# Kernel tuning notes

Hardware: AMD Instinct MI355X
Metric: run time of the kernel (lower is better)

## Reference

```python
import jax, jax.numpy as jnp
import numpy as np

EPS = 1e-8
TEMP = 0.2
HOPS = 2


def _inv_sqrt_deg(deg):
    # deg^-0.5 with inf -> 0 (isolated nodes)
    return jnp.where(deg > 0, jax.lax.rsqrt(jnp.maximum(deg, 1.0)) * jnp.where(deg > 0, 1.0, 0.0), 0.0)


def gcn_conv(h, u, v, W, b, n):
    # PyG GCNConv: add self-loops, symmetric normalization, aggr='add'
    h = h @ W  # [N, out]
    loops = jnp.arange(n, dtype=u.dtype)
    uu = jnp.concatenate([u, loops])
    vv = jnp.concatenate([v, loops])
    deg = jax.ops.segment_sum(jnp.ones_like(vv, dtype=h.dtype), vv, num_segments=n)
    dis = _inv_sqrt_deg(deg)
    norm = dis[uu] * dis[vv]  # [E+N]
    out = jax.ops.segment_sum(norm[:, None] * h[uu], vv, num_segments=n)
    return out + b


def compute_message_passing(u, v, x, n, hop=HOPS):
    # to_undirected: concat edges with their flips; remove self-loops via mask
    uu = jnp.concatenate([u, v])
    vv = jnp.concatenate([v, u])
    mask = (uu != vv).astype(x.dtype)
    deg = jax.ops.segment_sum(mask, vv, num_segments=n)
    dis = _inv_sqrt_deg(deg)
    norm = dis[uu] * dis[vv] * mask  # zero out self-loop edges
    for _ in range(hop):
        x = jax.ops.segment_sum(norm[:, None] * x[uu], vv, num_segments=n)
    return x


def _cos_sim(a, b):
    na = jnp.maximum(jnp.sqrt(jnp.sum(a * a, axis=-1)), EPS)
    nb = jnp.maximum(jnp.sqrt(jnp.sum(b * b, axis=-1)), EPS)
    return jnp.sum(a * b, axis=-1) / (na * nb)


def setup_inputs() -> dict:
    key = jax.random.key(0)
    ks = jax.random.split(key, 10)
    N, E, B = 100_000, 800_000, 100_000
    Din, H, Dout = 256, 256, 64
    x = jax.random.normal(ks[0], (N, Din), dtype=jnp.float32)
    src = jax.random.randint(ks[1], (E,), 0, N, dtype=jnp.int32)
    off = jax.random.randint(ks[2], (E,), 1, N, dtype=jnp.int32)
    dst = (src + off) % N  # guaranteed no self-loops
    edge_index = jnp.stack([src, dst])  # [2, E]
    batch = jax.random.randint(ks[3], (B, 3), 0, N, dtype=jnp.int32)
    s1, s2, sp = 1.0 / np.sqrt(Din), 1.0 / np.sqrt(H), 1.0 / np.sqrt(H)
    W1 = jax.random.normal(ks[4], (Din, H), dtype=jnp.float32) * s1
    b1 = jnp.zeros((H,), jnp.float32)
    W2 = jax.random.normal(ks[5], (H, H), dtype=jnp.float32) * s2
    b2 = jnp.zeros((H,), jnp.float32)
    Wp = jax.random.normal(ks[6], (H, Dout), dtype=jnp.float32) * sp
    bp = jnp.zeros((Dout,), jnp.float32)
    return {"x": x, "edge_index": edge_index, "batch": batch,
            "W1": W1, "b1": b1, "W2": W2, "b2": b2, "Wp": Wp, "bp": bp}


def reference(x, edge_index, batch, W1, b1, W2, b2, Wp, bp):
    n = x.shape[0]
    u, v = edge_index[0], edge_index[1]
    # gnn_encoder: 2-layer GCN
    h = jax.nn.relu(gcn_conv(x, u, v, W1, b1, n))
    h = gcn_conv(h, u, v, W2, b2, n)
    # graph_pred_linear
    node_emb = h @ Wp + bp  # [N, Dout]
    # 2-hop degree-normalized propagation on the undirected graph
    all_emb = compute_message_passing(u, v, node_emb, n)
    anc = all_emb[batch[:, 0]]
    pos = all_emb[batch[:, 1]]
    neg = all_emb[batch[:, 2]]
    xs = jnp.exp(_cos_sim(anc, pos) / TEMP)
    ys = jnp.exp(_cos_sim(anc, neg) / TEMP)
    loss = -jnp.log(xs / (xs + ys))
    return loss.mean()
```

## Files before the change

kernel.cpp:

```cpp
#include <hip/hip_runtime.h>
#include <hip/hip_bf16.h>

#define DIN 256
#define HID 256
#define DOUT 64
#define NPART 8
#define FPB 128
#define CCAP 32

typedef short short8 __attribute__((ext_vector_type(8)));
typedef float f32x4 __attribute__((ext_vector_type(4)));
typedef float f32x2 __attribute__((ext_vector_type(2)));

__device__ __forceinline__ float b2f(ushort u) {
    unsigned int x = ((unsigned int)u) << 16;
    return __builtin_bit_cast(float, x);
}
__device__ __forceinline__ ushort f2bf(float f) {
    unsigned int u = __builtin_bit_cast(unsigned int, f);
    unsigned int r = (u + 0x7FFFu + ((u >> 16) & 1u)) >> 16;
    return (ushort)r;
}
__device__ __forceinline__ unsigned int cvt_pk(float lo, float hi) {
    unsigned int r;
    asm("v_cvt_pk_bf16_f32 %0, %1, %2" : "=v"(r) : "v"(lo), "v"(hi));
    return r;
}
__device__ __forceinline__ unsigned char f2fp8(float v) {
    int p = __builtin_amdgcn_cvt_pk_fp8_f32(v, v, 0, false);
    return (unsigned char)(p & 0xff);
}
__device__ __forceinline__ ushort f2fp8x2(float lo, float hi) {
    int p = __builtin_amdgcn_cvt_pk_fp8_f32(lo, hi, 0, false);
    return (ushort)(p & 0xffff);
}
__device__ __forceinline__ void gload16(const void* g, void* l) {
    __builtin_amdgcn_global_load_lds(
        (const __attribute__((address_space(1))) unsigned int*)g,
        (__attribute__((address_space(3))) unsigned int*)l, 16, 0, 0);
}
__device__ __forceinline__ int swz8(int lane, int r) {
    return (((lane >> 1) ^ (r & 7)) << 4) + (lane & 1) * 8;
}

__device__ __forceinline__ void fill_body(int fid,
                                          const int* __restrict__ u,
                                          const int* __restrict__ v,
                                          int* __restrict__ cnt_in,
                                          int* __restrict__ cnt_out,
                                          int* __restrict__ col_in,
                                          int* __restrict__ col_out,
                                          int E, unsigned pdiv) {
    const int part = fid & (NPART - 1);
    const int step = FPB * 512;
    int e = (fid >> 3) * 512 + threadIdx.x;

#define PROC(aa, bb)                                                  \
    do {                                                              \
        if ((unsigned)(bb) / pdiv == (unsigned)part) {                \
            int s_ = atomicAdd(&cnt_in[bb], 1);                       \
            if (s_ < CCAP) col_in[(bb) * CCAP + s_] = (aa);           \
        }                                                             \
        if ((unsigned)(aa) / pdiv == (unsigned)part) {                \
            int s_ = atomicAdd(&cnt_out[aa], 1);                      \
            if (s_ < CCAP) col_out[(aa) * CCAP + s_] = (bb);          \
        }                                                             \
    } while (0)

    for (; e + 3 * step < E; e += 4 * step) {
        int a0 = u[e],            b0 = v[e];
        int a1 = u[e + step],     b1 = v[e + step];
        int a2 = u[e + 2 * step], b2 = v[e + 2 * step];
        int a3 = u[e + 3 * step], b3 = v[e + 3 * step];
        PROC(a0, b0);
        PROC(a1, b1);
        PROC(a2, b2);
        PROC(a3, b3);
    }
    for (; e < E; e += step) {
        int a = u[e], b = v[e];
        PROC(a, b);
    }
#undef PROC
}

template <int NT, int TN, int OUTMODE, bool ADD_BIAS, bool A_F32, bool SCALE>
__device__ __forceinline__ void gemm_body(
    int bidx, char* As, char* Bs,
    const void* __restrict__ A, const char* __restrict__ Bt,
    const float* __restrict__ bias, const float* __restrict__ rowscale,
    void* __restrict__ C, int M) {
    constexpr int BM = 64;
    constexpr int TILES = NT / TN;
    constexpr int FM = (TN == 128) ? 2 : 1;
    constexpr int FN = 2;
    const int tid = threadIdx.x;
    const int w = tid >> 6;
    const int lane = tid & 63;
    const int row0 = bidx * BM;
    const int wrow = (TN == 128) ? ((w >> 2) * 32) : ((w >> 1) * 16);
    const int wcol = (TN == 128) ? ((w & 3) * 32) : ((w & 1) * 32);
    const int g = lane >> 4;
    const int r15 = lane & 15;
    const int wb = w * 1024;

    if (A_F32) {
        const float* Af = (const float*)A;
        int r = tid >> 3;
        int c8 = tid & 7;
        int gr = row0 + r;
        gr = (gr < M) ? gr : (M - 1);
        const float* src = Af + (size_t)gr * 256 + c8 * 8;
#pragma unroll
        for (int k = 0; k < 4; ++k) {
            float4 f0 = *(const float4*)(src + k * 64);
            float4 f1 = *(const float4*)(src + k * 64 + 4);
            uint4 pv;
            pv.x = cvt_pk(f0.x, f0.y);
            pv.y = cvt_pk(f0.z, f0.w);
            pv.z = cvt_pk(f1.x, f1.y);
            pv.w = cvt_pk(f1.z, f1.w);
            int chunk = (c8 + 8 * k) ^ (r & 7);
            *(uint4*)(As + r * 512 + (chunk << 4)) = pv;
        }
    } else {
        const char* gA = (const char*)A + (size_t)row0 * 512;
#pragma unroll
        for (int i = 0; i < BM / 16; ++i)
            gload16(gA + i * 8192 + wb + lane * 16, As + i * 8192 + wb);
    }
    {
        const char* gB = Bt;
#pragma unroll
        for (int i = 0; i < TN / 16; ++i)
            gload16(gB + i * 8192 + wb + lane * 16, Bs + i * 8192 + wb);
    }

#pragma unroll
    for (int t = 0; t < TILES; ++t) {
        __syncthreads();

        f32x4 acc[FM][FN];
#pragma unroll
        for (int m = 0; m < FM; ++m)
#pragma unroll
            for (int n = 0; n < FN; ++n) acc[m][n] = {0.f, 0.f, 0.f, 0.f};

#pragma unroll
        for (int ks = 0; ks < 8; ++ks) {
            short8 a[FM], b[FN];
#pragma unroll
            for (int m = 0; m < FM; ++m) {
                int rl = wrow + m * 16 + r15;
                a[m] = *(const short8*)(As + rl * 512 + (((ks * 4 + g) ^ (rl & 7)) << 4));
            }
#pragma unroll
            for (int n = 0; n < FN; ++n) {
                int cl = wcol + n * 16 + r15;
                b[n] = *(const short8*)(Bs + cl * 512 + (((ks * 4 + g) ^ (cl & 7)) << 4));
            }
#pragma unroll
            for (int m = 0; m < FM; ++m)
#pragma unroll
                for (int n = 0; n < FN; ++n)
                    acc[m][n] = __builtin_amdgcn_mfma_f32_16x16x32_bf16(a[m], b[n], acc[m][n], 0, 0, 0);
        }

        __syncthreads();
        if (t + 1 < TILES) {
            const char* gB = Bt + (size_t)((t + 1) * TN) * 512;
#pragma unroll
            for (int i = 0; i < TN / 16; ++i)
                gload16(gB + i * 8192 + wb + lane * 16, Bs + i * 8192 + wb);
        }

#pragma unroll
        for (int m = 0; m < FM; ++m) {
            int rbase = row0 + wrow + m * 16 + g * 4;
#pragma unroll
            for (int j = 0; j < 4; ++j) {
                int grow = rbase + j;
                if (grow >= M) continue;
                float rs = SCALE ? rowscale[grow] : 1.0f;
#pragma unroll
                for (int n = 0; n < FN; ++n) {
                    int gcol = t * TN + wcol + n * 16 + r15;
                    float vv = acc[m][n][j];
                    if (ADD_BIAS) vv += bias[gcol];
                    if (SCALE) vv *= rs;
                    if (OUTMODE == 2)
                        ((unsigned char*)C)[(size_t)grow * 256 + gcol] = f2fp8(vv);
                    else
                        ((unsigned char*)C)[(size_t)grow * 64 + gcol] = f2fp8(vv);
                }
            }
        }
    }
}

__global__ __launch_bounds__(512) void fill_gemm1_kernel(
    const int* __restrict__ u, const int* __restrict__ v,
    int* __restrict__ cnt_in, int* __restrict__ cnt_out,
    int* __restrict__ col_in, int* __restrict__ col_out,
    int E, unsigned pdiv,
    const float* __restrict__ x, const char* __restrict__ w1t,
    unsigned char* __restrict__ hb, int M,
    int gG, int gF, int nG, int nF) {
    __shared__ __align__(16) char As[64 * 512];
    __shared__ __align__(16) char Bs[64 * 512];
    const int G = blockIdx.x >> 3;
    const int sub = blockIdx.x & 7;
    const int gmin = (gG < gF) ? gG : gF;
    bool isG;
    int idx;
    if (G < 2 * gmin) {
        isG = ((G & 1) == 0);
        idx = (G >> 1) * 8 + sub;
    } else if (gG > gF) {
        isG = true;
        idx = (G - gmin) * 8 + sub;
    } else {
        isG = false;
        idx = (G - gmin) * 8 + sub;
    }
    if (isG) {
        if (idx < nG)
            gemm_body<256, 64, 2, false, true, false>(idx, As, Bs, x, w1t,
                                                      nullptr, nullptr, hb, M);
    } else {
        if (idx < nF)
            fill_body(idx, u, v, cnt_in, cnt_out, col_in, col_out, E, pdiv);
    }
}

template <int NT, int TN, int OUTMODE, bool ADD_BIAS, bool A_F32>
__global__ __launch_bounds__(512) void mfma_gemm_v7(
    const void* __restrict__ A, const char* __restrict__ Bt,
    const float* __restrict__ bias, const float* __restrict__ rowscale,
    void* __restrict__ C, int M) {
    __shared__ __align__(16) char As[64 * 512];
    __shared__ __align__(16) char Bs[TN * 512];
    gemm_body<NT, TN, OUTMODE, ADD_BIAS, A_F32, true>(
        blockIdx.x, As, Bs, A, Bt, bias, rowscale, C, M);
}

__global__ __launch_bounds__(256) void wprep_kernel(
    const float* __restrict__ W1, const float* __restrict__ W2,
    const float* __restrict__ Wp, const float* __restrict__ b2,
    const float* __restrict__ bp,
    char* __restrict__ w1t, char* __restrict__ wct, float* __restrict__ c2) {
    int blk = blockIdx.x;
    int k = threadIdx.x;
    if (blk < 256) {
        int row = blk;
        *(ushort*)(w1t + (size_t)row * 512 + (((k >> 3) ^ (row & 7)) << 4) + (k & 7) * 2)
            = f2bf(W1[k * 256 + row]);
        return;
    }
    if (blk < 320) {
        int c = blk - 256;
        const float* w2row = W2 + (size_t)k * 256;
        float s0 = 0.f, s1 = 0.f, s2 = 0.f, s3 = 0.f;
        float s4 = 0.f, s5 = 0.f, s6 = 0.f, s7 = 0.f;
#pragma unroll 4
        for (int j = 0; j < 256; j += 8) {
            s0 += w2row[j + 0] * Wp[(j + 0) * 64 + c];
            s1 += w2row[j + 1] * Wp[(j + 1) * 64 + c];
            s2 += w2row[j + 2] * Wp[(j + 2) * 64 + c];
            s3 += w2row[j + 3] * Wp[(j + 3) * 64 + c];
            s4 += w2row[j + 4] * Wp[(j + 4) * 64 + c];
            s5 += w2row[j + 5] * Wp[(j + 5) * 64 + c];
            s6 += w2row[j + 6] * Wp[(j + 6) * 64 + c];
            s7 += w2row[j + 7] * Wp[(j + 7) * 64 + c];
        }
        float dot = ((s0 + s1) + (s2 + s3)) + ((s4 + s5) + (s6 + s7));
        *(ushort*)(wct + (size_t)c * 512 + (((k >> 3) ^ (c & 7)) << 4) + (k & 7) * 2)
            = f2bf(dot);
        return;
    }
    if (k < 64) {
        float s = 0.f;
        for (int j = 0; j < 256; ++j) s += b2[j] * Wp[j * 64 + k];
        c2[k] = s + bp[k];
    }
}

__global__ __launch_bounds__(256) void dis_kernel(const int* __restrict__ cnt_in,
                                                  const int* __restrict__ cnt_out,
                                                  float* __restrict__ dis_g,
                                                  float* __restrict__ dis_m,
                                                  int N) {
    int i = blockIdx.x * blockDim.x + threadIdx.x;
    if (i >= N) return;
    int ci = cnt_in[i];
    dis_g[i] = rsqrtf((float)ci + 1.0f);
    int dm = ci + cnt_out[i];
    dis_m[i] = (dm > 0) ? rsqrtf((float)dm) : 0.0f;
}

__global__ __launch_bounds__(256) void conv_gather_fp8(const unsigned char* __restrict__ h,
                                                       const float* __restrict__ dis,
                                                       const float* __restrict__ bias,
                                                       const int* __restrict__ cnt_in,
                                                       const int* __restrict__ col_in,
                                                       char* __restrict__ out,
                                                       int N) {
    int wid = (blockIdx.x * blockDim.x + threadIdx.x) >> 6;
    int lane = threadIdx.x & 63;
    if (wid >= N) return;
    float di = dis[wid];
    float a0, a1, a2, a3;
    {
        unsigned q = *(const unsigned*)(h + (size_t)wid * 256 + lane * 4);
        f32x2 lo = __builtin_amdgcn_cvt_pk_f32_fp8((int)q, false);
        f32x2 hi = __builtin_amdgcn_cvt_pk_f32_fp8((int)q, true);
        a0 = di * lo.x; a1 = di * lo.y; a2 = di * hi.x; a3 = di * hi.y;
    }
    const int* list = col_in + (size_t)wid * CCAP;
    int cnt = cnt_in[wid];
    cnt = (cnt < CCAP) ? cnt : CCAP;
    int e = 0;
    for (; e + 7 < cnt; e += 8) {
        int ss[8];
        unsigned qs[8];
#pragma unroll
        for (int k = 0; k < 8; ++k) ss[k] = list[e + k];
#pragma unroll
        for (int k = 0; k < 8; ++k)
            qs[k] = *(const unsigned*)(h + (size_t)ss[k] * 256 + lane * 4);
#pragma unroll
        for (int k = 0; k < 8; ++k) {
            float wgt = dis[ss[k]];
            f32x2 lo = __builtin_amdgcn_cvt_pk_f32_fp8((int)qs[k], false);
            f32x2 hi = __builtin_amdgcn_cvt_pk_f32_fp8((int)qs[k], true);
            a0 += wgt * lo.x; a1 += wgt * lo.y;
            a2 += wgt * hi.x; a3 += wgt * hi.y;
        }
    }
    for (; e < cnt; ++e) {
        int s = list[e];
        float wgt = dis[s];
        unsigned q = *(const unsigned*)(h + (size_t)s * 256 + lane * 4);
        f32x2 lo = __builtin_amdgcn_cvt_pk_f32_fp8((int)q, false);
        f32x2 hi = __builtin_amdgcn_cvt_pk_f32_fp8((int)q, true);
        a0 += wgt * lo.x; a1 += wgt * lo.y;
        a2 += wgt * hi.x; a3 += wgt * hi.y;
    }
    float4 bv = ((const float4*)bias)[lane];
    float o0 = fmaxf(di * a0 + bv.x, 0.f);
    float o1 = fmaxf(di * a1 + bv.y, 0.f);
    float o2 = fmaxf(di * a2 + bv.z, 0.f);
    float o3 = fmaxf(di * a3 + bv.w, 0.f);
    uint2 ov;
    ov.x = cvt_pk(o0, o1);
    ov.y = cvt_pk(o2, o3);
    *(uint2*)(out + (size_t)wid * 512 + swz8(lane, wid)) = ov;
}

__global__ __launch_bounds__(256) void conv2proj_gather(const unsigned char* __restrict__ q,
                                                        const float* __restrict__ dis_g,
                                                        const float* __restrict__ dis_m,
                                                        const float* __restrict__ c2,
                                                        const int* __restrict__ cnt_in,
                                                        const int* __restrict__ col_in,
                                                        unsigned char* __restrict__ out,
                                                        int N) {
    int wid = (blockIdx.x * blockDim.x + threadIdx.x) >> 6;
    int lane = threadIdx.x & 63;
    if (wid >= N) return;
    const int half = lane >> 5;
    const int l2 = lane & 31;
    const int* list = col_in + (size_t)wid * CCAP;
    int cnt = cnt_in[wid];
    cnt = (cnt < CCAP) ? cnt : CCAP;
    float a0 = 0.f, a1 = 0.f;
    int e = half;
    for (; e + 6 < cnt; e += 8) {
        int s0 = list[e], s1 = list[e + 2], s2 = list[e + 4], s3 = list[e + 6];
        ushort q0 = *(const ushort*)(q + (size_t)s0 * 64 + l2 * 2);
        ushort q1 = *(const ushort*)(q + (size_t)s1 * 64 + l2 * 2);
        ushort q2 = *(const ushort*)(q + (size_t)s2 * 64 + l2 * 2);
        ushort q3 = *(const ushort*)(q + (size_t)s3 * 64 + l2 * 2);
        f32x2 f0 = __builtin_amdgcn_cvt_pk_f32_fp8((int)q0, false);
        f32x2 f1 = __builtin_amdgcn_cvt_pk_f32_fp8((int)q1, false);
        f32x2 f2 = __builtin_amdgcn_cvt_pk_f32_fp8((int)q2, false);
        f32x2 f3 = __builtin_amdgcn_cvt_pk_f32_fp8((int)q3, false);
        a0 += f0.x + f1.x + f2.x + f3.x;
        a1 += f0.y + f1.y + f2.y + f3.y;
    }
    for (; e < cnt; e += 2) {
        int s = list[e];
        ushort qq = *(const ushort*)(q + (size_t)s * 64 + l2 * 2);
        f32x2 f = __builtin_amdgcn_cvt_pk_f32_fp8((int)qq, false);
        a0 += f.x;
        a1 += f.y;
    }
    if (half == 0) {
        ushort qq = *(const ushort*)(q + (size_t)wid * 64 + l2 * 2);
        f32x2 f = __builtin_amdgcn_cvt_pk_f32_fp8((int)qq, false);
        a0 += f.x;
        a1 += f.y;
    }
    a0 += __shfl_xor(a0, 32);
    a1 += __shfl_xor(a1, 32);
    if (half == 0) {
        float dg = dis_g[wid], dm = dis_m[wid];
        float cA = c2[l2 * 2], cB = c2[l2 * 2 + 1];
        *(ushort*)(out + (size_t)wid * 64 + l2 * 2) =
            f2fp8x2(dm * (dg * a0 + cA), dm * (dg * a1 + cB));
    }
}

template <int POW>
__global__ __launch_bounds__(256) void mp_gather_fp8(const unsigned char* __restrict__ in,
                                                     const float* __restrict__ dis,
                                                     const int* __restrict__ cnt_in,
                                                     const int* __restrict__ cnt_out,
                                                     const int* __restrict__ col_in,
                                                     const int* __restrict__ col_out,
                                                     unsigned char* __restrict__ out,
                                                     int N) {
    int wid = (blockIdx.x * blockDim.x + threadIdx.x) >> 6;
    int lane = threadIdx.x & 63;
    if (wid >= N) return;
    const int half = lane >> 5;
    const int l2 = lane & 31;
    const int* list;
    int cnt;
    if (half == 0) {
        list = col_in + (size_t)wid * CCAP;
        cnt = cnt_in[wid];
    } else {
        list = col_out + (size_t)wid * CCAP;
        cnt = cnt_out[wid];
    }
    cnt = (cnt < CCAP) ? cnt : CCAP;
    float a0 = 0.f, a1 = 0.f;
    int e = 0;
    for (; e + 3 < cnt; e += 4) {
        int s0 = list[e], s1 = list[e + 1], s2 = list[e + 2], s3 = list[e + 3];
        ushort q0 = *(const ushort*)(in + (size_t)s0 * 64 + l2 * 2);
        ushort q1 = *(const ushort*)(in + (size_t)s1 * 64 + l2 * 2);
        ushort q2 = *(const ushort*)(in + (size_t)s2 * 64 + l2 * 2);
        ushort q3 = *(const ushort*)(in + (size_t)s3 * 64 + l2 * 2);
        f32x2 f0 = __builtin_amdgcn_cvt_pk_f32_fp8((int)q0, false);
        f32x2 f1 = __builtin_amdgcn_cvt_pk_f32_fp8((int)q1, false);
        f32x2 f2 = __builtin_amdgcn_cvt_pk_f32_fp8((int)q2, false);
        f32x2 f3 = __builtin_amdgcn_cvt_pk_f32_fp8((int)q3, false);
        a0 += f0.x + f1.x + f2.x + f3.x;
        a1 += f0.y + f1.y + f2.y + f3.y;
    }
    for (; e < cnt; ++e) {
        int s = list[e];
        ushort q = *(const ushort*)(in + (size_t)s * 64 + l2 * 2);
        f32x2 f = __builtin_amdgcn_cvt_pk_f32_fp8((int)q, false);
        a0 += f.x;
        a1 += f.y;
    }
    a0 += __shfl_xor(a0, 32);
    a1 += __shfl_xor(a1, 32);
    if (half == 0) {
        float d = dis[wid];
        float sc = (POW == 2) ? d * d : d;
        *(ushort*)(out + (size_t)wid * 64 + l2 * 2) = f2fp8x2(sc * a0, sc * a1);
    }
}

__global__ __launch_bounds__(256) void loss_kernel(const unsigned char* __restrict__ emb,
                                                   const int* __restrict__ batch,
                                                   float* __restrict__ out,
                                                   int B, float invB) {
    const int nhw = gridDim.x * 8;
    const int hwid = blockIdx.x * 8 + (threadIdx.x >> 5);
    const int l2 = threadIdx.x & 31;
    float lsum = 0.0f;
    for (int r = hwid; r < B; r += nhw) {
        int a = batch[r * 3 + 0];
        int p = batch[r * 3 + 1];
        int ng = batch[r * 3 + 2];
        ushort qa = *(const ushort*)(emb + (size_t)a * 64 + l2 * 2);
        ushort qp = *(const ushort*)(emb + (size_t)p * 64 + l2 * 2);
        ushort qn = *(const ushort*)(emb + (size_t)ng * 64 + l2 * 2);
        f32x2 fa = __builtin_amdgcn_cvt_pk_f32_fp8((int)qa, false);
        f32x2 fp = __builtin_amdgcn_cvt_pk_f32_fp8((int)qp, false);
        f32x2 fn = __builtin_amdgcn_cvt_pk_f32_fp8((int)qn, false);
        float aa = fa.x * fa.x + fa.y * fa.y;
        float pp = fp.x * fp.x + fp.y * fp.y;
        float nn = fn.x * fn.x + fn.y * fn.y;
        float ap = fa.x * fp.x + fa.y * fp.y;
        float an = fa.x * fn.x + fa.y * fn.y;
#pragma unroll
        for (int off = 16; off > 0; off >>= 1) {
            aa += __shfl_xor(aa, off);
            pp += __shfl_xor(pp, off);
            nn += __shfl_xor(nn, off);
            ap += __shfl_xor(ap, off);
            an += __shfl_xor(an, off);
        }
        if (l2 == 0) {
            float na = fmaxf(sqrtf(aa), 1e-8f);
            float npp = fmaxf(sqrtf(pp), 1e-8f);
            float nnn = fmaxf(sqrtf(nn), 1e-8f);
            float cx = ap / (na * npp);
            float cy = an / (na * nnn);
            lsum += log1pf(expf((cy - cx) * 5.0f));
        }
    }
    __shared__ float part[8];
    if (l2 == 0) part[threadIdx.x >> 5] = lsum;
    __syncthreads();
    if (threadIdx.x == 0) {
        float s = 0.f;
#pragma unroll
        for (int i = 0; i < 8; ++i) s += part[i];
        atomicAdd(out, s * invB);
    }
}

extern "C" void kernel_launch(void* const* d_in, const int* in_sizes, int n_in,
                              void* d_out, int out_size, void* d_ws, size_t ws_size,
                              hipStream_t stream) {
    const float* x   = (const float*)d_in[0];
    const int* ei    = (const int*)d_in[1];
    const int* batch = (const int*)d_in[2];
    const float* W1  = (const float*)d_in[3];
    const float* b1  = (const float*)d_in[4];
    const float* W2  = (const float*)d_in[5];
    const float* b2  = (const float*)d_in[6];
    const float* Wp  = (const float*)d_in[7];
    const float* bp  = (const float*)d_in[8];
    const int N = in_sizes[0] / DIN;
    const int E = in_sizes[1] / 2;
    const int B = in_sizes[2] / 3;
    const int* u = ei;
    const int* v = ei + E;
    const unsigned pdiv = (unsigned)((N + NPART - 1) / NPART);

    char* aggb    = (char*)d_ws;
    unsigned char* hb = (unsigned char*)(aggb + (size_t)N * 512);
    unsigned char* embA = hb + (size_t)N * 256;
    unsigned char* embB = embA + (size_t)N * 64;
    char* w1t     = (char*)(embB + (size_t)N * 64);
    char* wct     = w1t + 256 * 512;
    float* c2     = (float*)(wct + 64 * 512);
    float* dis_g  = c2 + 64;
    float* dis_m  = dis_g + N;
    int* cnt_in   = (int*)(dis_m + N);
    int* cnt_out  = cnt_in + N;
    int* col_in   = cnt_out + N;
    int* col_out  = col_in + (size_t)N * CCAP;

    const int nwb = (N + 3) / 4;
    const int ndisb = (N + 255) / 256;
    const int gm = (N + 63) / 64;

    hipMemsetAsync(cnt_in, 0, 2 * (size_t)N * sizeof(int), stream);
    wprep_kernel<<<321, 256, 0, stream>>>(W1, W2, Wp, b2, bp, w1t, wct, c2);

    const int nG = gm;
    const int gG = (nG + 7) / 8;
    const int nF = NPART * FPB;
    const int gF = nF / 8;
    fill_gemm1_kernel<<<(gG + gF) * 8, 512, 0, stream>>>(
        u, v, cnt_in, cnt_out, col_in, col_out, E, pdiv,
        x, w1t, hb, N, gG, gF, nG, nF);

    dis_kernel<<<ndisb, 256, 0, stream>>>(cnt_in, cnt_out, dis_g, dis_m, N);

    conv_gather_fp8<<<nwb, 256, 0, stream>>>(hb, dis_g, b1, cnt_in, col_in, aggb, N);

    mfma_gemm_v7<64, 64, 3, false, false><<<gm, 512, 0, stream>>>(
        aggb, wct, nullptr, dis_g, embB, N);

    conv2proj_gather<<<nwb, 256, 0, stream>>>(embB, dis_g, dis_m, c2,
                                              cnt_in, col_in, embA, N);

    mp_gather_fp8<2><<<nwb, 256, 0, stream>>>(embA, dis_m, cnt_in, cnt_out,
                                              col_in, col_out, embB, N);
    mp_gather_fp8<1><<<nwb, 256, 0, stream>>>(embB, dis_m, cnt_in, cnt_out,
                                              col_in, col_out, embA, N);

    hipMemsetAsync(d_out, 0, sizeof(float), stream);
    loss_kernel<<<1024, 256, 0, stream>>>(embA, batch, (float*)d_out, B, 1.0f / (float)B);
}
```

Measured before the change: 372.8 us.

## Compute degree norms on the fly and fold weight prep into fill kernel

Removes the separate dis_kernel and computes rsqrt degree normalizations inline from the count arrays in each gather kernel. The W2·Wp product and bias prep move into extra blocks of the fill/GEMM1 launch, leaving a smaller W1 cast kernel. The row scaling after GEMM2 is moved into conv2proj_gather's per-neighbor weights, so the GEMM epilogue is simpler. Together these drop launches and the dis arrays, at the cost of extra count loads and rsqrt calls in the gathers and a shallower unroll in conv2proj.

```diff
diff --git a/kernel.cpp b/kernel.cpp
--- a/kernel.cpp
+++ b/kernel.cpp
@@ -84,11 +84,10 @@
 #undef PROC
 }
 
-template <int NT, int TN, int OUTMODE, bool ADD_BIAS, bool A_F32, bool SCALE>
+template <int NT, int TN, int OUTMODE, bool A_F32>
 __device__ __forceinline__ void gemm_body(
     int bidx, char* As, char* Bs,
     const void* __restrict__ A, const char* __restrict__ Bt,
-    const float* __restrict__ bias, const float* __restrict__ rowscale,
     void* __restrict__ C, int M) {
     constexpr int BM = 64;
     constexpr int TILES = NT / TN;
@@ -181,13 +180,10 @@
             for (int j = 0; j < 4; ++j) {
                 int grow = rbase + j;
                 if (grow >= M) continue;
-                float rs = SCALE ? rowscale[grow] : 1.0f;
 #pragma unroll
                 for (int n = 0; n < FN; ++n) {
                     int gcol = t * TN + wcol + n * 16 + r15;
                     float vv = acc[m][n][j];
-                    if (ADD_BIAS) vv += bias[gcol];
-                    if (SCALE) vv *= rs;
                     if (OUTMODE == 2)
                         ((unsigned char*)C)[(size_t)grow * 256 + gcol] = f2fp8(vv);
                     else
@@ -205,9 +201,43 @@
     int E, unsigned pdiv,
     const float* __restrict__ x, const char* __restrict__ w1t,
     unsigned char* __restrict__ hb, int M,
+    const float* __restrict__ W2, const float* __restrict__ Wp,
+    const float* __restrict__ b2, const float* __restrict__ bp,
+    char* __restrict__ wct, float* __restrict__ c2,
     int gG, int gF, int nG, int nF) {
     __shared__ __align__(16) char As[64 * 512];
     __shared__ __align__(16) char Bs[64 * 512];
+    const int mainB = (gG + gF) * 8;
+    if ((int)blockIdx.x >= mainB) {
+        int pidx = blockIdx.x - mainB;
+        int k = threadIdx.x & 255;
+        if (pidx < 32) {
+            int c = pidx * 2 + (threadIdx.x >> 8);
+            const float* w2row = W2 + (size_t)k * 256;
+            float s0 = 0.f, s1 = 0.f, s2 = 0.f, s3 = 0.f;
+            float s4 = 0.f, s5 = 0.f, s6 = 0.f, s7 = 0.f;
+#pragma unroll 4
+            for (int j = 0; j < 256; j += 8) {
+                s0 += w2row[j + 0] * Wp[(j + 0) * 64 + c];
+                s1 += w2row[j + 1] * Wp[(j + 1) * 64 + c];
+                s2 += w2row[j + 2] * Wp[(j + 2) * 64 + c];
+                s3 += w2row[j + 3] * Wp[(j + 3) * 64 + c];
+                s4 += w2row[j + 4] * Wp[(j + 4) * 64 + c];
+                s5 += w2row[j + 5] * Wp[(j + 5) * 64 + c];
+                s6 += w2row[j + 6] * Wp[(j + 6) * 64 + c];
+                s7 += w2row[j + 7] * Wp[(j + 7) * 64 + c];
+            }
+            float dot = ((s0 + s1) + (s2 + s3)) + ((s4 + s5) + (s6 + s7));
+            *(ushort*)(wct + (size_t)c * 512 + (((k >> 3) ^ (c & 7)) << 4) + (k & 7) * 2)
+                = f2bf(dot);
+        } else if (threadIdx.x < 64) {
+            int c = threadIdx.x;
+            float s = 0.f;
+            for (int j = 0; j < 256; ++j) s += b2[j] * Wp[j * 64 + c];
+            c2[c] = s + bp[c];
+        }
+        return;
+    }
     const int G = blockIdx.x >> 3;
     const int sub = blockIdx.x & 7;
     const int gmin = (gG < gF) ? gG : gF;
@@ -225,81 +255,31 @@
     }
     if (isG) {
         if (idx < nG)
-            gemm_body<256, 64, 2, false, true, false>(idx, As, Bs, x, w1t,
-                                                      nullptr, nullptr, hb, M);
+            gemm_body<256, 64, 2, true>(idx, As, Bs, x, w1t, hb, M);
     } else {
         if (idx < nF)
             fill_body(idx, u, v, cnt_in, cnt_out, col_in, col_out, E, pdiv);
     }
 }
 
-template <int NT, int TN, int OUTMODE, bool ADD_BIAS, bool A_F32>
-__global__ __launch_bounds__(512) void mfma_gemm_v7(
+template <int NT, int TN, int OUTMODE>
+__global__ __launch_bounds__(512) void mfma_gemm_v8(
     const void* __restrict__ A, const char* __restrict__ Bt,
-    const float* __restrict__ bias, const float* __restrict__ rowscale,
     void* __restrict__ C, int M) {
     __shared__ __align__(16) char As[64 * 512];
     __shared__ __align__(16) char Bs[TN * 512];
-    gemm_body<NT, TN, OUTMODE, ADD_BIAS, A_F32, true>(
-        blockIdx.x, As, Bs, A, Bt, bias, rowscale, C, M);
-}
-
-__global__ __launch_bounds__(256) void wprep_kernel(
-    const float* __restrict__ W1, const float* __restrict__ W2,
-    const float* __restrict__ Wp, const float* __restrict__ b2,
-    const float* __restrict__ bp,
-    char* __restrict__ w1t, char* __restrict__ wct, float* __restrict__ c2) {
-    int blk = blockIdx.x;
+    gemm_body<NT, TN, OUTMODE, false>(blockIdx.x, As, Bs, A, Bt, C, M);
+}
+
+__global__ __launch_bounds__(256) void wcast1_kernel(const float* __restrict__ W1,
+                                                     char* __restrict__ w1t) {
+    int row = blockIdx.x;
     int k = threadIdx.x;
-    if (blk < 256) {
-        int row = blk;
-        *(ushort*)(w1t + (size_t)row * 512 + (((k >> 3) ^ (row & 7)) << 4) + (k & 7) * 2)
-            = f2bf(W1[k * 256 + row]);
-        return;
-    }
-    if (blk < 320) {
-        int c = blk - 256;
-        const float* w2row = W2 + (size_t)k * 256;
-        float s0 = 0.f, s1 = 0.f, s2 = 0.f, s3 = 0.f;
-        float s4 = 0.f, s5 = 0.f, s6 = 0.f, s7 = 0.f;
-#pragma unroll 4
-        for (int j = 0; j < 256; j += 8) {
-            s0 += w2row[j + 0] * Wp[(j + 0) * 64 + c];
-            s1 += w2row[j + 1] * Wp[(j + 1) * 64 + c];
-            s2 += w2row[j + 2] * Wp[(j + 2) * 64 + c];
-            s3 += w2row[j + 3] * Wp[(j + 3) * 64 + c];
-            s4 += w2row[j + 4] * Wp[(j + 4) * 64 + c];
-            s5 += w2row[j + 5] * Wp[(j + 5) * 64 + c];
-            s6 += w2row[j + 6] * Wp[(j + 6) * 64 + c];
-            s7 += w2row[j + 7] * Wp[(j + 7) * 64 + c];
-        }
-        float dot = ((s0 + s1) + (s2 + s3)) + ((s4 + s5) + (s6 + s7));
-        *(ushort*)(wct + (size_t)c * 512 + (((k >> 3) ^ (c & 7)) << 4) + (k & 7) * 2)
-            = f2bf(dot);
-        return;
-    }
-    if (k < 64) {
-        float s = 0.f;
-        for (int j = 0; j < 256; ++j) s += b2[j] * Wp[j * 64 + k];
-        c2[k] = s + bp[k];
-    }
-}
-
-__global__ __launch_bounds__(256) void dis_kernel(const int* __restrict__ cnt_in,
-                                                  const int* __restrict__ cnt_out,
-                                                  float* __restrict__ dis_g,
-                                                  float* __restrict__ dis_m,
-                                                  int N) {
-    int i = blockIdx.x * blockDim.x + threadIdx.x;
-    if (i >= N) return;
-    int ci = cnt_in[i];
-    dis_g[i] = rsqrtf((float)ci + 1.0f);
-    int dm = ci + cnt_out[i];
-    dis_m[i] = (dm > 0) ? rsqrtf((float)dm) : 0.0f;
+    *(ushort*)(w1t + (size_t)row * 512 + (((k >> 3) ^ (row & 7)) << 4) + (k & 7) * 2)
+        = f2bf(W1[k * 256 + row]);
 }
 
 __global__ __launch_bounds__(256) void conv_gather_fp8(const unsigned char* __restrict__ h,
-                                                       const float* __restrict__ dis,
                                                        const float* __restrict__ bias,
                                                        const int* __restrict__ cnt_in,
                                                        const int* __restrict__ col_in,
@@ -308,7 +288,9 @@
     int wid = (blockIdx.x * blockDim.x + threadIdx.x) >> 6;
     int lane = threadIdx.x & 63;
     if (wid >= N) return;
-    float di = dis[wid];
+    int cnt = cnt_in[wid];
+    float di = rsqrtf((float)cnt + 1.0f);
+    cnt = (cnt < CCAP) ? cnt : CCAP;
     float a0, a1, a2, a3;
     {
         unsigned q = *(const unsigned*)(h + (size_t)wid * 256 + lane * 4);
@@ -317,8 +299,6 @@
         a0 = di * lo.x; a1 = di * lo.y; a2 = di * hi.x; a3 = di * hi.y;
     }
     const int* list = col_in + (size_t)wid * CCAP;
-    int cnt = cnt_in[wid];
-    cnt = (cnt < CCAP) ? cnt : CCAP;
     int e = 0;
     for (; e + 7 < cnt; e += 8) {
         int ss[8];
@@ -330,7 +310,7 @@
             qs[k] = *(const unsigned*)(h + (size_t)ss[k] * 256 + lane * 4);
 #pragma unroll
         for (int k = 0; k < 8; ++k) {
-            float wgt = dis[ss[k]];
+            float wgt = rsqrtf((float)cnt_in[ss[k]] + 1.0f);
             f32x2 lo = __builtin_amdgcn_cvt_pk_f32_fp8((int)qs[k], false);
             f32x2 hi = __builtin_amdgcn_cvt_pk_f32_fp8((int)qs[k], true);
             a0 += wgt * lo.x; a1 += wgt * lo.y;
@@ -339,7 +319,7 @@
     }
     for (; e < cnt; ++e) {
         int s = list[e];
-        float wgt = dis[s];
+        float wgt = rsqrtf((float)cnt_in[s] + 1.0f);
         unsigned q = *(const unsigned*)(h + (size_t)s * 256 + lane * 4);
         f32x2 lo = __builtin_amdgcn_cvt_pk_f32_fp8((int)q, false);
         f32x2 hi = __builtin_amdgcn_cvt_pk_f32_fp8((int)q, true);
@@ -358,10 +338,9 @@
 }
 
 __global__ __launch_bounds__(256) void conv2proj_gather(const unsigned char* __restrict__ q,
-                                                        const float* __restrict__ dis_g,
-                                                        const float* __restrict__ dis_m,
                                                         const float* __restrict__ c2,
                                                         const int* __restrict__ cnt_in,
+                                                        const int* __restrict__ cnt_out,
                                                         const int* __restrict__ col_in,
                                                         unsigned char* __restrict__ out,
                                                         int N) {
@@ -370,41 +349,42 @@
     if (wid >= N) return;
     const int half = lane >> 5;
     const int l2 = lane & 31;
+    int ci = cnt_in[wid];
+    float dg = rsqrtf((float)ci + 1.0f);
+    int cnt = (ci < CCAP) ? ci : CCAP;
     const int* list = col_in + (size_t)wid * CCAP;
-    int cnt = cnt_in[wid];
-    cnt = (cnt < CCAP) ? cnt : CCAP;
     float a0 = 0.f, a1 = 0.f;
     int e = half;
-    for (; e + 6 < cnt; e += 8) {
-        int s0 = list[e], s1 = list[e + 2], s2 = list[e + 4], s3 = list[e + 6];
+    for (; e + 2 < cnt; e += 4) {
+        int s0 = list[e], s1 = list[e + 2];
+        float w0 = rsqrtf((float)cnt_in[s0] + 1.0f);
+        float w1 = rsqrtf((float)cnt_in[s1] + 1.0f);
         ushort q0 = *(const ushort*)(q + (size_t)s0 * 64 + l2 * 2);
         ushort q1 = *(const ushort*)(q + (size_t)s1 * 64 + l2 * 2);
-        ushort q2 = *(const ushort*)(q + (size_t)s2 * 64 + l2 * 2);
-        ushort q3 = *(const ushort*)(q + (size_t)s3 * 64 + l2 * 2);
         f32x2 f0 = __builtin_amdgcn_cvt_pk_f32_fp8((int)q0, false);
         f32x2 f1 = __builtin_amdgcn_cvt_pk_f32_fp8((int)q1, false);
-        f32x2 f2 = __builtin_amdgcn_cvt_pk_f32_fp8((int)q2, false);
-        f32x2 f3 = __builtin_amdgcn_cvt_pk_f32_fp8((int)q3, false);
-        a0 += f0.x + f1.x + f2.x + f3.x;
-        a1 += f0.y + f1.y + f2.y + f3.y;
+        a0 += w0 * f0.x + w1 * f1.x;
+        a1 += w0 * f0.y + w1 * f1.y;
     }
     for (; e < cnt; e += 2) {
         int s = list[e];
+        float w = rsqrtf((float)cnt_in[s] + 1.0f);
         ushort qq = *(const ushort*)(q + (size_t)s * 64 + l2 * 2);
         f32x2 f = __builtin_amdgcn_cvt_pk_f32_fp8((int)qq, false);
-        a0 += f.x;
-        a1 += f.y;
+        a0 += w * f.x;
+        a1 += w * f.y;
     }
     if (half == 0) {
         ushort qq = *(const ushort*)(q + (size_t)wid * 64 + l2 * 2);
         f32x2 f = __builtin_amdgcn_cvt_pk_f32_fp8((int)qq, false);
-        a0 += f.x;
-        a1 += f.y;
+        a0 += dg * f.x;
+        a1 += dg * f.y;
     }
     a0 += __shfl_xor(a0, 32);
     a1 += __shfl_xor(a1, 32);
     if (half == 0) {
-        float dg = dis_g[wid], dm = dis_m[wid];
+        int dmc = ci + cnt_out[wid];
+        float dm = (dmc > 0) ? rsqrtf((float)dmc) : 0.0f;
         float cA = c2[l2 * 2], cB = c2[l2 * 2 + 1];
         *(ushort*)(out + (size_t)wid * 64 + l2 * 2) =
             f2fp8x2(dm * (dg * a0 + cA), dm * (dg * a1 + cB));
@@ -413,7 +393,6 @@
 
 template <int POW>
 __global__ __launch_bounds__(256) void mp_gather_fp8(const unsigned char* __restrict__ in,
-                                                     const float* __restrict__ dis,
                                                      const int* __restrict__ cnt_in,
                                                      const int* __restrict__ cnt_out,
                                                      const int* __restrict__ col_in,
@@ -427,12 +406,14 @@
     const int l2 = lane & 31;
     const int* list;
     int cnt;
+    int ci = cnt_in[wid];
+    int co = cnt_out[wid];
     if (half == 0) {
         list = col_in + (size_t)wid * CCAP;
-        cnt = cnt_in[wid];
+        cnt = ci;
     } else {
         list = col_out + (size_t)wid * CCAP;
-        cnt = cnt_out[wid];
+        cnt = co;
     }
     cnt = (cnt < CCAP) ? cnt : CCAP;
     float a0 = 0.f, a1 = 0.f;
@@ -460,7 +441,8 @@
     a0 += __shfl_xor(a0, 32);
     a1 += __shfl_xor(a1, 32);
     if (half == 0) {
-        float d = dis[wid];
+        int dmc = ci + co;
+        float d = (dmc > 0) ? rsqrtf((float)dmc) : 0.0f;
         float sc = (POW == 2) ? d * d : d;
         *(ushort*)(out + (size_t)wid * 64 + l2 * 2) = f2fp8x2(sc * a0, sc * a1);
     }
@@ -543,41 +525,35 @@
     char* w1t     = (char*)(embB + (size_t)N * 64);
     char* wct     = w1t + 256 * 512;
     float* c2     = (float*)(wct + 64 * 512);
-    float* dis_g  = c2 + 64;
-    float* dis_m  = dis_g + N;
-    int* cnt_in   = (int*)(dis_m + N);
+    int* cnt_in   = (int*)(c2 + 64);
     int* cnt_out  = cnt_in + N;
     int* col_in   = cnt_out + N;
     int* col_out  = col_in + (size_t)N * CCAP;
 
     const int nwb = (N + 3) / 4;
-    const int ndisb = (N + 255) / 256;
     const int gm = (N + 63) / 64;
 
     hipMemsetAsync(cnt_in, 0, 2 * (size_t)N * sizeof(int), stream);
-    wprep_kernel<<<321, 256, 0, stream>>>(W1, W2, Wp, b2, bp, w1t, wct, c2);
+    wcast1_kernel<<<256, 256, 0, stream>>>(W1, w1t);
 
     const int nG = gm;
     const int gG = (nG + 7) / 8;
     const int nF = NPART * FPB;
     const int gF = nF / 8;
-    fill_gemm1_kernel<<<(gG + gF) * 8, 512, 0, stream>>>(
+    fill_gemm1_kernel<<<(gG + gF) * 8 + 33, 512, 0, stream>>>(
         u, v, cnt_in, cnt_out, col_in, col_out, E, pdiv,
-        x, w1t, hb, N, gG, gF, nG, nF);
-
-    dis_kernel<<<ndisb, 256, 0, stream>>>(cnt_in, cnt_out, dis_g, dis_m, N);
-
-    conv_gather_fp8<<<nwb, 256, 0, stream>>>(hb, dis_g, b1, cnt_in, col_in, aggb, N);
-
-    mfma_gemm_v7<64, 64, 3, false, false><<<gm, 512, 0, stream>>>(
-        aggb, wct, nullptr, dis_g, embB, N);
-
-    conv2proj_gather<<<nwb, 256, 0, stream>>>(embB, dis_g, dis_m, c2,
-                                              cnt_in, col_in, embA, N);
-
-    mp_gather_fp8<2><<<nwb, 256, 0, stream>>>(embA, dis_m, cnt_in, cnt_out,
+        x, w1t, hb, N, W2, Wp, b2, bp, wct, c2, gG, gF, nG, nF);
+
+    conv_gather_fp8<<<nwb, 256, 0, stream>>>(hb, b1, cnt_in, col_in, aggb, N);
+
+    mfma_gemm_v8<64, 64, 3><<<gm, 512, 0, stream>>>(aggb, wct, embB, N);
+
+    conv2proj_gather<<<nwb, 256, 0, stream>>>(embB, c2, cnt_in, cnt_out,
+                                              col_in, embA, N);
+
+    mp_gather_fp8<2><<<nwb, 256, 0, stream>>>(embA, cnt_in, cnt_out,
                                               col_in, col_out, embB, N);
-    mp_gather_fp8<1><<<nwb, 256, 0, stream>>>(embB, dis_m, cnt_in, cnt_out,
+    mp_gather_fp8<1><<<nwb, 256, 0, stream>>>(embB, cnt_in, cnt_out,
                                               col_in, col_out, embA, N);
 
     hipMemsetAsync(d_out, 0, sizeof(float), stream);
```

Result: no change. 372.1 us (-0.2%).
